# Kernel optimization log

Hardware: AMD Instinct MI355X
Metric: run time of the kernel (lower is better)

Reference implementation:

```python
import jax, jax.numpy as jnp
import numpy as np

Nt, Nr, Mt, Mr, G, N_r_RF, num_sc = 64, 64, 32, 32, 64, 4, 32
B = 64
R = Mr // N_r_RF  # number of RF-chain blocks


def setup_inputs() -> dict:
    key = jax.random.key(0)
    k0, k1, k2, k3, k4 = jax.random.split(key, 5)
    return {
        "H_real_imag": jax.random.normal(k0, (B, Nr, Nt, num_sc, 2), jnp.float32),
        "noise_real_imag": jax.random.normal(k1, (B, R, Nr, Mt * num_sc, 2), jnp.float32),
        "kernel_W": jax.random.normal(k2, (Nr, Mr), jnp.float32),
        "kernel_F": jax.random.normal(k3, (Nt, Mt), jnp.float32),
        "kernel_Kron2": jax.random.normal(k4, (Nt * Nr, G * G, 2), jnp.float32),
    }


def reference(H_real_imag, noise_real_imag, kernel_W, kernel_F, kernel_Kron2):
    # Unit-modulus analog combiner / precoder from phases
    W = ((jnp.cos(kernel_W) + 1j * jnp.sin(kernel_W)) / np.float32(np.sqrt(Nr))).astype(jnp.complex64)  # (Nr, Mr)
    F = ((jnp.cos(kernel_F) + 1j * jnp.sin(kernel_F)) / np.float32(np.sqrt(Nt))).astype(jnp.complex64)  # (Nt, Mt)

    # Q = kron(F^T, W^H): (Mt*Mr, Nt*Nr)
    Q = jnp.kron(F.T, W.conj().T)

    Kron2 = (kernel_Kron2[..., 0] + 1j * kernel_Kron2[..., 1]).astype(jnp.complex64)  # (Nt*Nr, G^2)
    Phi = Q @ Kron2  # (Mt*Mr, G^2)
    Phi_real_imag = jnp.stack([Phi.real, Phi.imag], axis=-1)  # (Mt*Mr, G^2, 2)

    # Effective noise: block-wise W_r^H @ n_r, vectorized over RF blocks
    noise = (noise_real_imag[..., 0] + 1j * noise_real_imag[..., 1]).astype(jnp.complex64)  # (B,R,Nr,Mt*S)
    Wb = W.reshape(Nr, R, N_r_RF)  # Wb[:, r, :] == W[:, r*k:(r+1)*k]
    eff = jnp.einsum('nrk,brnx->brkx', Wb.conj(), noise)  # (B,R,k,Mt*S)
    eff = eff.reshape(-1, Mr, Mt, num_sc)

    # Measurements: y = Q vec(H^T) + n, batched over all subcarriers at once
    H = (H_real_imag[..., 0] + 1j * H_real_imag[..., 1]).astype(jnp.complex64)  # (B,Nr,Nt,S)
    h = jnp.transpose(H, (0, 2, 1, 3)).reshape(-1, Nt * Nr, num_sc)  # (B, Nt*Nr, S)
    n = jnp.transpose(eff, (0, 2, 1, 3)).reshape(-1, Mt * Mr, num_sc)  # (B, Mt*Mr, S)
    y = jnp.einsum('qn,bns->bqs', Q, h) + n  # (B, Mt*Mr, S)
    y_real_imag = jnp.stack([y.real, y.imag], axis=-1)  # (B, Mt*Mr, S, 2)

    return Phi_real_imag, y_real_imag
```

## Files before the change

### kernel.cpp

```cpp
#include <hip/hip_runtime.h>
#include <hip/hip_bf16.h>

typedef unsigned short u16;
typedef unsigned int u32;

#define WS_CONJW 0
#define WS_F     4096
#define WS_FLAG  8192

__device__ __forceinline__ float bfb2f(u16 b){
  union { u32 u; float f; } v; v.u = ((u32)b) << 16; return v.f;
}
__device__ __forceinline__ float2 ldc(const void* p, long i, bool bf){
  if (bf){ ushort2 v = ((const ushort2*)p)[i]; return make_float2(bfb2f(v.x), bfb2f(v.y)); }
  return ((const float2*)p)[i];
}
__device__ __forceinline__ float lds1(const void* p, int i, bool bf){
  return bf ? bfb2f(((const u16*)p)[i]) : ((const float*)p)[i];
}
__device__ __forceinline__ bool detect_bf16(const void* kW){
  const u32* p = (const u32*)kW;
  int hits = 0;
  for (int i = 0; i < 64; ++i){
    int e = (p[i] >> 7) & 0xFF;
    hits += (e >= 100 && e <= 140) ? 1 : 0;
  }
  return hits >= 48;
}

__global__ void wf_kernel(const void* __restrict__ kW, const void* __restrict__ kF,
                          float* __restrict__ ws){
  const bool bf = detect_bf16(kW);
  int t = blockIdx.x * 256 + threadIdx.x;
  if (t == 0) ws[WS_FLAG] = bf ? 1.0f : 0.0f;
  if (t < 2048){
    float w = lds1(kW, t, bf);
    ws[WS_CONJW + 2*t]     =  cosf(w) * 0.125f;
    ws[WS_CONJW + 2*t + 1] = -sinf(w) * 0.125f;
  } else if (t < 4096){
    int i = t - 2048;
    float f = lds1(kF, i, bf);
    ws[WS_F + 2*i]     = cosf(f) * 0.125f;
    ws[WS_F + 2*i + 1] = sinf(f) * 0.125f;
  }
}

__global__ __launch_bounds__(256) void eff_kernel(const void* __restrict__ noise,
                                                  const float* __restrict__ ws,
                                                  float2* __restrict__ y2){
  const bool bf = ws[WS_FLAG] != 0.0f;
  const int bid = blockIdx.x;
  const int b   = bid >> 4;
  const int xc  = (bid >> 2) & 3;
  const int mrq = bid & 3;
  const int x   = (xc << 8) + threadIdx.x;
  const int r0  = mrq << 1;
  float ar[8], ai[8];
#pragma unroll
  for (int j = 0; j < 8; ++j){ ar[j] = 0.f; ai[j] = 0.f; }
  for (int nr = 0; nr < 64; ++nr){
    long i0 = ((long)((b*8 + r0    )*64 + nr) << 10) + x;
    long i1 = ((long)((b*8 + r0 + 1)*64 + nr) << 10) + x;
    float2 n0 = ldc(noise, i0, bf);
    float2 n1 = ldc(noise, i1, bf);
#pragma unroll
    for (int j = 0; j < 8; ++j){
      int mr = (mrq << 3) + j;
      float wr = ws[WS_CONJW + (nr*32 + mr)*2];
      float wi = ws[WS_CONJW + (nr*32 + mr)*2 + 1];
      float xr = (j < 4) ? n0.x : n1.x;
      float xi = (j < 4) ? n0.y : n1.y;
      ar[j] += wr*xr - wi*xi;
      ai[j] += wr*xi + wi*xr;
    }
  }
  const int mt = x >> 5, s = x & 31;
#pragma unroll
  for (int j = 0; j < 8; ++j){
    int mr = (mrq << 3) + j;
    long o = ((long)((b << 10) + (mt << 5) + mr) << 5) + s;
    y2[o] = make_float2(ar[j], ai[j]);
  }
}

__global__ __launch_bounds__(256) void uy_kernel(const void* __restrict__ H,
                                                 const float* __restrict__ ws,
                                                 float2* __restrict__ y2){
  __shared__ float cw[4096];
  __shared__ float hs[8192];
  __shared__ float tm[32*65*2];
  const bool bf = ws[WS_FLAG] != 0.0f;
  const int b = blockIdx.x >> 5;
  const int s = blockIdx.x & 31;
  const int t = threadIdx.x;
  for (int i = t; i < 4096; i += 256) cw[i] = ws[WS_CONJW + i];
#pragma unroll
  for (int k = 0; k < 16; ++k){
    int p  = t + (k << 8);
    long i = ((long)(((b << 6) + (p >> 6)) << 6) + (p & 63)) * 32 + s;
    float2 v = ldc(H, i, bf);
    hs[2*p] = v.x; hs[2*p + 1] = v.y;
  }
  __syncthreads();
  {
    const int mr = t & 31, ntg = t >> 5;
    float tr[8], ti[8];
#pragma unroll
    for (int j = 0; j < 8; ++j){ tr[j] = 0.f; ti[j] = 0.f; }
    for (int nr = 0; nr < 64; ++nr){
      float wr = cw[(nr*32 + mr)*2];
      float wi = cw[(nr*32 + mr)*2 + 1];
#pragma unroll
      for (int j = 0; j < 8; ++j){
        int nt = (ntg << 3) + j;
        float hr = hs[(nr*64 + nt)*2];
        float hi = hs[(nr*64 + nt)*2 + 1];
        tr[j] += wr*hr - wi*hi;
        ti[j] += wr*hi + wi*hr;
      }
    }
#pragma unroll
    for (int j = 0; j < 8; ++j){
      int nt = (ntg << 3) + j;
      tm[(mr*65 + nt)*2]     = tr[j];
      tm[(mr*65 + nt)*2 + 1] = ti[j];
    }
  }
  __syncthreads();
  {
    const int mr = t & 31, mtg = t >> 5;
    float yr[4], yi[4];
#pragma unroll
    for (int j = 0; j < 4; ++j){ yr[j] = 0.f; yi[j] = 0.f; }
    for (int nt = 0; nt < 64; ++nt){
      float Tr = tm[(mr*65 + nt)*2];
      float Ti = tm[(mr*65 + nt)*2 + 1];
#pragma unroll
      for (int j = 0; j < 4; ++j){
        int mt = (mtg << 2) + j;
        float fr = ws[WS_F + (nt*32 + mt)*2];
        float fi = ws[WS_F + (nt*32 + mt)*2 + 1];
        yr[j] += fr*Tr - fi*Ti;
        yi[j] += fr*Ti + fi*Tr;
      }
    }
#pragma unroll
    for (int j = 0; j < 4; ++j){
      int mt = (mtg << 2) + j;
      long o = ((long)((b << 10) + (mt << 5) + mr) << 5) + s;
      float2 e = y2[o];
      y2[o] = make_float2(yr[j] + e.x, yi[j] + e.y);
    }
  }
}

__global__ __launch_bounds__(256) void phi_kernel(const void* __restrict__ K2,
                                                  const float* __restrict__ ws,
                                                  float2* __restrict__ phi2){
  __shared__ float cw[4096];
  __shared__ float k2s[1024];
  const bool bf = ws[WS_FLAG] != 0.0f;
  const int t = threadIdx.x;
  for (int i = t; i < 4096; i += 256) cw[i] = ws[WS_CONJW + i];
  const int g  = t & 7;
  const int mr = t >> 3;
  const int g0 = blockIdx.x << 3;
  const int lr = t >> 2;
  const int lp = (t & 3) << 1;
  float accr[32], acci[32];
#pragma unroll
  for (int mt = 0; mt < 32; ++mt){ accr[mt] = 0.f; acci[mt] = 0.f; }
  __syncthreads();
  for (int nt = 0; nt < 64; ++nt){
    long base = (long)(nt*64 + lr) * 4096 + g0 + lp;
    float4 vv;
    if (bf){
      ushort4 v = *(const ushort4*)((const u16*)K2 + 2*base);
      vv = make_float4(bfb2f(v.x), bfb2f(v.y), bfb2f(v.z), bfb2f(v.w));
    } else {
      vv = *(const float4*)((const float*)K2 + 2*base);
    }
    k2s[(lr*8 + lp)*2    ] = vv.x;
    k2s[(lr*8 + lp)*2 + 1] = vv.y;
    k2s[(lr*8 + lp)*2 + 2] = vv.z;
    k2s[(lr*8 + lp)*2 + 3] = vv.w;
    __syncthreads();
    float sr = 0.f, si = 0.f;
#pragma unroll
    for (int nr = 0; nr < 64; ++nr){
      float wr = cw[(nr*32 + mr)*2];
      float wi = cw[(nr*32 + mr)*2 + 1];
      float kr = k2s[(nr*8 + g)*2];
      float ki = k2s[(nr*8 + g)*2 + 1];
      sr += wr*kr - wi*ki;
      si += wr*ki + wi*kr;
    }
#pragma unroll
    for (int mt = 0; mt < 32; ++mt){
      float fr = ws[WS_F + (nt*32 + mt)*2];
      float fi = ws[WS_F + (nt*32 + mt)*2 + 1];
      accr[mt] += fr*sr - fi*si;
      acci[mt] += fr*si + fi*sr;
    }
    __syncthreads();
  }
#pragma unroll
  for (int mt = 0; mt < 32; ++mt){
    long o = (long)((mt << 5) + mr) * 4096 + g0 + g;
    phi2[o] = make_float2(accr[mt], acci[mt]);
  }
}

extern "C" void kernel_launch(void* const* d_in, const int* in_sizes, int n_in,
                              void* d_out, int out_size, void* d_ws, size_t ws_size,
                              hipStream_t stream) {
  const void* H     = d_in[0];
  const void* noise = d_in[1];
  const void* kW    = d_in[2];
  const void* kF    = d_in[3];
  const void* K2    = d_in[4];
  float* out = (float*)d_out;
  float* ws = (float*)d_ws;

  float2* phi2 = (float2*)out;
  float2* y2   = (float2*)(out + 8388608);

  wf_kernel <<<16,   256, 0, stream>>>(kW, kF, ws);
  eff_kernel<<<1024, 256, 0, stream>>>(noise, ws, y2);
  uy_kernel <<<2048, 256, 0, stream>>>(H, ws, y2);
  phi_kernel<<<512,  256, 0, stream>>>(K2, ws, phi2);
}
```

Measured before the change: 878.6 us.

## Split Phi into two register-tiled passes through a workspace intermediate

The single shared-memory Phi kernel is replaced by two kernels when the workspace is large enough. The first computes S = W^H·Kron2 for each nt and stores it in the workspace. The second applies F to S to produce Phi, with each thread holding 32 accumulators and reading the W/F coefficients as uniform loads. This removes the per-nt LDS staging and block barriers and raises parallelism, at the cost of writing and then reading a 64 MB intermediate. The eff kernel also gains software prefetching of noise two iterations ahead.

```diff
diff --git a/kernel.cpp b/kernel.cpp
--- a/kernel.cpp
+++ b/kernel.cpp
@@ -7,6 +7,8 @@
 #define WS_CONJW 0
 #define WS_F     4096
 #define WS_FLAG  8192
+#define WS_S     16384
+#define WS_NEED  ((size_t)(16384 + 64*32*4096*2) * 4)
 
 __device__ __forceinline__ float bfb2f(u16 b){
   union { u32 u; float f; } v; v.u = ((u32)b) << 16; return v.f;
@@ -14,6 +16,11 @@
 __device__ __forceinline__ float2 ldc(const void* p, long i, bool bf){
   if (bf){ ushort2 v = ((const ushort2*)p)[i]; return make_float2(bfb2f(v.x), bfb2f(v.y)); }
   return ((const float2*)p)[i];
+}
+__device__ __forceinline__ float4 ldc2(const void* p, long i, bool bf){
+  if (bf){ ushort4 v = *(const ushort4*)((const u16*)p + 2*i);
+           return make_float4(bfb2f(v.x), bfb2f(v.y), bfb2f(v.z), bfb2f(v.w)); }
+  return *(const float4*)((const float*)p + 2*i);
 }
 __device__ __forceinline__ float lds1(const void* p, int i, bool bf){
   return bf ? bfb2f(((const u16*)p)[i]) : ((const float*)p)[i];
@@ -58,18 +65,27 @@
   float ar[8], ai[8];
 #pragma unroll
   for (int j = 0; j < 8; ++j){ ar[j] = 0.f; ai[j] = 0.f; }
+  const long base0 = ((long)((b*8 + r0    )*64) << 10) + x;
+  const long base1 = ((long)((b*8 + r0 + 1)*64) << 10) + x;
+  float2 c0 = ldc(noise, base0, bf);
+  float2 c1 = ldc(noise, base1, bf);
+  float2 n0 = ldc(noise, base0 + 1024, bf);
+  float2 n1 = ldc(noise, base1 + 1024, bf);
+#pragma unroll 2
   for (int nr = 0; nr < 64; ++nr){
-    long i0 = ((long)((b*8 + r0    )*64 + nr) << 10) + x;
-    long i1 = ((long)((b*8 + r0 + 1)*64 + nr) << 10) + x;
-    float2 n0 = ldc(noise, i0, bf);
-    float2 n1 = ldc(noise, i1, bf);
+    const float2 f0 = c0, f1 = c1;
+    c0 = n0; c1 = n1;
+    if (nr < 62){
+      n0 = ldc(noise, base0 + ((long)(nr + 2) << 10), bf);
+      n1 = ldc(noise, base1 + ((long)(nr + 2) << 10), bf);
+    }
 #pragma unroll
     for (int j = 0; j < 8; ++j){
       int mr = (mrq << 3) + j;
       float wr = ws[WS_CONJW + (nr*32 + mr)*2];
       float wi = ws[WS_CONJW + (nr*32 + mr)*2 + 1];
-      float xr = (j < 4) ? n0.x : n1.x;
-      float xi = (j < 4) ? n0.y : n1.y;
+      float xr = (j < 4) ? f0.x : f1.x;
+      float xi = (j < 4) ? f0.y : f1.y;
       ar[j] += wr*xr - wi*xi;
       ai[j] += wr*xi + wi*xr;
     }
@@ -154,9 +170,66 @@
   }
 }
 
-__global__ __launch_bounds__(256) void phi_kernel(const void* __restrict__ K2,
-                                                  const float* __restrict__ ws,
-                                                  float2* __restrict__ phi2){
+__global__ __launch_bounds__(256) void s_kernel(const void* __restrict__ K2,
+                                                const float* __restrict__ ws,
+                                                float2* __restrict__ S){
+  const bool bf = ws[WS_FLAG] != 0.0f;
+  const int nt = blockIdx.x >> 4;
+  const int g  = ((blockIdx.x & 15) << 8) + threadIdx.x;
+  const long base0 = ((long)nt << 18) + g;
+  float accr[32], acci[32];
+#pragma unroll
+  for (int mr = 0; mr < 32; ++mr){ accr[mr] = 0.f; acci[mr] = 0.f; }
+  float2 c  = ldc(K2, base0, bf);
+  float2 nx = ldc(K2, base0 + 4096, bf);
+  for (int nr = 0; nr < 64; ++nr){
+    const float2 k = c; c = nx;
+    if (nr < 62) nx = ldc(K2, base0 + ((long)(nr + 2) << 12), bf);
+#pragma unroll
+    for (int mr = 0; mr < 32; ++mr){
+      float wr = ws[WS_CONJW + (nr*32 + mr)*2];
+      float wi = ws[WS_CONJW + (nr*32 + mr)*2 + 1];
+      accr[mr] += wr*k.x - wi*k.y;
+      acci[mr] += wr*k.y + wi*k.x;
+    }
+  }
+#pragma unroll
+  for (int mr = 0; mr < 32; ++mr)
+    S[((long)(nt*32 + mr) << 12) + g] = make_float2(accr[mr], acci[mr]);
+}
+
+__global__ __launch_bounds__(256) void p2_kernel(const float2* __restrict__ S,
+                                                 const float* __restrict__ ws,
+                                                 float2* __restrict__ phi2){
+  const int mr = blockIdx.x >> 4;
+  const int g  = ((blockIdx.x & 15) << 8) + threadIdx.x;
+  const long base0 = ((long)mr << 12) + g;
+  float accr[32], acci[32];
+#pragma unroll
+  for (int mt = 0; mt < 32; ++mt){ accr[mt] = 0.f; acci[mt] = 0.f; }
+  float2 c  = S[base0];
+  float2 nx = S[base0 + (1L << 17)];
+  for (int nt = 0; nt < 64; ++nt){
+    const float2 s = c; c = nx;
+    if (nt < 62) nx = S[base0 + ((long)(nt + 2) << 17)];
+#pragma unroll
+    for (int mt = 0; mt < 32; ++mt){
+      float fr = ws[WS_F + (nt*32 + mt)*2];
+      float fi = ws[WS_F + (nt*32 + mt)*2 + 1];
+      accr[mt] += fr*s.x - fi*s.y;
+      acci[mt] += fr*s.y + fi*s.x;
+    }
+  }
+#pragma unroll
+  for (int mt = 0; mt < 32; ++mt){
+    long o = (long)((mt << 5) + mr) * 4096 + g;
+    phi2[o] = make_float2(accr[mt], acci[mt]);
+  }
+}
+
+__global__ __launch_bounds__(256) void phi_fallback(const void* __restrict__ K2,
+                                                    const float* __restrict__ ws,
+                                                    float2* __restrict__ phi2){
   __shared__ float cw[4096];
   __shared__ float k2s[1024];
   const bool bf = ws[WS_FLAG] != 0.0f;
@@ -173,13 +246,7 @@
   __syncthreads();
   for (int nt = 0; nt < 64; ++nt){
     long base = (long)(nt*64 + lr) * 4096 + g0 + lp;
-    float4 vv;
-    if (bf){
-      ushort4 v = *(const ushort4*)((const u16*)K2 + 2*base);
-      vv = make_float4(bfb2f(v.x), bfb2f(v.y), bfb2f(v.z), bfb2f(v.w));
-    } else {
-      vv = *(const float4*)((const float*)K2 + 2*base);
-    }
+    float4 vv = ldc2(K2, base, bf);
     k2s[(lr*8 + lp)*2    ] = vv.x;
     k2s[(lr*8 + lp)*2 + 1] = vv.y;
     k2s[(lr*8 + lp)*2 + 2] = vv.z;
@@ -228,5 +295,11 @@
   wf_kernel <<<16,   256, 0, stream>>>(kW, kF, ws);
   eff_kernel<<<1024, 256, 0, stream>>>(noise, ws, y2);
   uy_kernel <<<2048, 256, 0, stream>>>(H, ws, y2);
-  phi_kernel<<<512,  256, 0, stream>>>(K2, ws, phi2);
-}
+  if (ws_size >= WS_NEED){
+    float2* S = (float2*)(ws + WS_S);
+    s_kernel <<<1024, 256, 0, stream>>>(K2, ws, S);
+    p2_kernel<<<512,  256, 0, stream>>>(S, ws, phi2);
+  } else {
+    phi_fallback<<<512, 256, 0, stream>>>(K2, ws, phi2);
+  }
+}
```

Measured after the change: 809.0 us. 7.9% less time.
